# Kernel optimization log

Measured on AMD Instinct MI355X. Metric: run time of the kernel, lower is better.

The kernel has to match this reference:

```python
import jax, jax.numpy as jnp
import numpy as np

EPS = 1e-5

def layer_norm(x, g, b):
    mu = jnp.mean(x, axis=-1, keepdims=True)
    var = jnp.var(x, axis=-1, keepdims=True)
    return (x - mu) * jax.lax.rsqrt(var + EPS) * g + b

def setup_inputs() -> dict:
    key = jax.random.key(0)
    ks = jax.random.split(key, 8)
    B, N, C, H = 4, 1024, 1024, 16
    Dh = C * 4
    std = 0.02
    return {
        "x": jax.random.normal(ks[0], (B, N, C), dtype=jnp.float32),
        "qkv_w": jax.random.normal(ks[1], (3 * C, C), dtype=jnp.float32) * std,
        "proj_w": jax.random.normal(ks[2], (C, C), dtype=jnp.float32) * std,
        "proj_b": jnp.zeros((C,), dtype=jnp.float32),
        "fc1_w": jax.random.normal(ks[3], (Dh, C), dtype=jnp.float32) * std,
        "fc1_b": jnp.zeros((Dh,), dtype=jnp.float32),
        "fc2_w": jax.random.normal(ks[4], (C, Dh), dtype=jnp.float32) * std,
        "fc2_b": jnp.zeros((C,), dtype=jnp.float32),
        "ln1_g": jnp.ones((C,), dtype=jnp.float32),
        "ln1_b": jnp.zeros((C,), dtype=jnp.float32),
        "ln2_g": jnp.ones((C,), dtype=jnp.float32),
        "ln2_b": jnp.zeros((C,), dtype=jnp.float32),
        "lnh_g": jnp.ones((Dh,), dtype=jnp.float32),
        "lnh_b": jnp.zeros((Dh,), dtype=jnp.float32),
    }

def reference(x, qkv_w, proj_w, proj_b, fc1_w, fc1_b, fc2_w, fc2_b,
              ln1_g, ln1_b, ln2_g, ln2_b, lnh_g, lnh_b):
    B, N, C = x.shape
    H = 16
    Dh = C // H
    scale = Dh ** (-0.5)

    # --- attention sublayer (pre-norm) ---
    h = layer_norm(x, ln1_g, ln1_b)
    qkv = (h @ qkv_w.T).reshape(B, N, 3, H, Dh).transpose(2, 0, 3, 1, 4)  # [3,B,H,N,Dh]
    q, k, v = qkv[0], qkv[1], qkv[2]
    attn = jnp.einsum('bhid,bhjd->bhij', q, k) * scale
    attn = jax.nn.softmax(attn, axis=-1)
    o = jnp.einsum('bhij,bhjd->bhid', attn, v)          # [B,H,N,Dh]
    o = o.transpose(0, 2, 1, 3).reshape(B, N, C)
    o = o @ proj_w.T + proj_b
    x = x + o

    # --- MLP sublayer (pre-norm, with LN on hidden per use_ln=True) ---
    h = layer_norm(x, ln2_g, ln2_b)
    u = jax.nn.gelu(h @ fc1_w.T + fc1_b, approximate=False)  # torch nn.GELU = erf form
    u = layer_norm(u, lnh_g, lnh_b)
    m = u @ fc2_w.T + fc2_b
    return x + m
```

## Files before the change

### kernel.cpp

```cpp
#include <hip/hip_runtime.h>
#include <hip/hip_bf16.h>
#include <math.h>


#define TOKENS 4096
#define CDIM   1024
#define HEADS  16
#define DHEAD  64
#define HID    4096

typedef __attribute__((ext_vector_type(4))) float  floatx4;
typedef __attribute__((ext_vector_type(8))) short  short8;

__device__ __forceinline__ void gl_lds16(const void* g, void* l)
{
    __builtin_amdgcn_global_load_lds(
        (const __attribute__((address_space(1))) unsigned int*)g,
        (__attribute__((address_space(3))) unsigned int*)l,
        16, 0, 0);
}

__global__ __launch_bounds__(256) void cvt_all(
    const float* __restrict__ s0, const float* __restrict__ s1,
    const float* __restrict__ s2, const float* __restrict__ s3,
    __hip_bfloat16* __restrict__ dst)
{
    long i = (long)blockIdx.x * 256 + threadIdx.x;
    const float* src;
    long base;
    if (i < 768l * 1024)       { src = s0; base = 0; }
    else if (i < 1792l * 1024) { src = s1; base = 768l * 1024; }
    else if (i < 2816l * 1024) { src = s2; base = 1792l * 1024; }
    else                       { src = s3; base = 2816l * 1024; }
    float4 v = ((const float4*)src)[i - base];
    __hip_bfloat16 t[4];
    t[0] = __float2bfloat16(v.x);
    t[1] = __float2bfloat16(v.y);
    t[2] = __float2bfloat16(v.z);
    t[3] = __float2bfloat16(v.w);
    *(uint2*)(dst + 4l * i) = *(uint2*)t;
}

__global__ __launch_bounds__(256) void ln_f32_kernel(
    const float* __restrict__ x, const float* __restrict__ g,
    const float* __restrict__ b, __hip_bfloat16* __restrict__ y, int C)
{
    int row = blockIdx.x;
    const float4* xr = (const float4*)(x + (long)row * C);
    uint2* yr = (uint2*)(y + (long)row * C);
    const int C4 = C >> 2;

    float s = 0.f, ss = 0.f;
    for (int i = threadIdx.x; i < C4; i += 256) {
        float4 v = xr[i];
        s  += v.x + v.y + v.z + v.w;
        ss += v.x * v.x + v.y * v.y + v.z * v.z + v.w * v.w;
    }
    #pragma unroll
    for (int d = 32; d; d >>= 1) {
        s  += __shfl_down(s, d);
        ss += __shfl_down(ss, d);
    }
    __shared__ float buf[4][2];
    int wid = threadIdx.x >> 6, lane = threadIdx.x & 63;
    if (lane == 0) { buf[wid][0] = s; buf[wid][1] = ss; }
    __syncthreads();
    if (threadIdx.x == 0) {
        s = buf[0][0] + buf[1][0] + buf[2][0] + buf[3][0];
        ss = buf[0][1] + buf[1][1] + buf[2][1] + buf[3][1];
        buf[0][0] = s; buf[0][1] = ss;
    }
    __syncthreads();
    s = buf[0][0]; ss = buf[0][1];

    float invC = 1.f / (float)C;
    float mu = s * invC;
    float var = ss * invC - mu * mu;
    float inv = rsqrtf(var + 1e-5f);
    const float4* gg = (const float4*)g;
    const float4* bb = (const float4*)b;
    for (int i = threadIdx.x; i < C4; i += 256) {
        float4 v = xr[i], gv = gg[i], bv = bb[i];
        __hip_bfloat16 t[4];
        t[0] = __float2bfloat16((v.x - mu) * inv * gv.x + bv.x);
        t[1] = __float2bfloat16((v.y - mu) * inv * gv.y + bv.y);
        t[2] = __float2bfloat16((v.z - mu) * inv * gv.z + bv.z);
        t[3] = __float2bfloat16((v.w - mu) * inv * gv.w + bv.w);
        yr[i] = *(uint2*)t;
    }
}

__global__ __launch_bounds__(256) void ln_bf16_kernel(
    const __hip_bfloat16* __restrict__ x, const float* __restrict__ g,
    const float* __restrict__ b, __hip_bfloat16* __restrict__ y, int C)
{
    int row = blockIdx.x;
    const uint4* xr = (const uint4*)(x + (long)row * C);
    uint4* yr = (uint4*)(y + (long)row * C);
    const int C8 = C >> 3;

    float s = 0.f, ss = 0.f;
    for (int i = threadIdx.x; i < C8; i += 256) {
        uint4 raw = xr[i];
        const __hip_bfloat16* p = (const __hip_bfloat16*)&raw;
        #pragma unroll
        for (int j = 0; j < 8; ++j) {
            float v = __bfloat162float(p[j]);
            s += v; ss += v * v;
        }
    }
    #pragma unroll
    for (int d = 32; d; d >>= 1) {
        s  += __shfl_down(s, d);
        ss += __shfl_down(ss, d);
    }
    __shared__ float buf[4][2];
    int wid = threadIdx.x >> 6, lane = threadIdx.x & 63;
    if (lane == 0) { buf[wid][0] = s; buf[wid][1] = ss; }
    __syncthreads();
    if (threadIdx.x == 0) {
        s = buf[0][0] + buf[1][0] + buf[2][0] + buf[3][0];
        ss = buf[0][1] + buf[1][1] + buf[2][1] + buf[3][1];
        buf[0][0] = s; buf[0][1] = ss;
    }
    __syncthreads();
    s = buf[0][0]; ss = buf[0][1];

    float invC = 1.f / (float)C;
    float mu = s * invC;
    float var = ss * invC - mu * mu;
    float inv = rsqrtf(var + 1e-5f);
    const float4* gg = (const float4*)g;
    const float4* bb = (const float4*)b;
    for (int i = threadIdx.x; i < C8; i += 256) {
        uint4 raw = xr[i];
        const __hip_bfloat16* p = (const __hip_bfloat16*)&raw;
        float4 g0 = gg[2 * i], g1 = gg[2 * i + 1];
        float4 b0 = bb[2 * i], b1 = bb[2 * i + 1];
        __hip_bfloat16 t[8];
        t[0] = __float2bfloat16((__bfloat162float(p[0]) - mu) * inv * g0.x + b0.x);
        t[1] = __float2bfloat16((__bfloat162float(p[1]) - mu) * inv * g0.y + b0.y);
        t[2] = __float2bfloat16((__bfloat162float(p[2]) - mu) * inv * g0.z + b0.z);
        t[3] = __float2bfloat16((__bfloat162float(p[3]) - mu) * inv * g0.w + b0.w);
        t[4] = __float2bfloat16((__bfloat162float(p[4]) - mu) * inv * g1.x + b1.x);
        t[5] = __float2bfloat16((__bfloat162float(p[5]) - mu) * inv * g1.y + b1.y);
        t[6] = __float2bfloat16((__bfloat162float(p[6]) - mu) * inv * g1.z + b1.z);
        t[7] = __float2bfloat16((__bfloat162float(p[7]) - mu) * inv * g1.w + b1.w);
        yr[i] = *(uint4*)t;
    }
}

template<int BK>
__global__ __launch_bounds__(256, BK == 64 ? 2 : 1) void gemm_db(
    const __hip_bfloat16* __restrict__ A,
    const __hip_bfloat16* __restrict__ W,
    const float* __restrict__ bias, const float* __restrict__ residual,
    void* __restrict__ Cout, int M, int N, int K, int mode)
{
    constexpr int ROWSEG = 512 / BK;
    constexpr int CHK    = BK / 8;
    constexpr int MASK   = CHK - 1;
    constexpr int NSEGW  = BK / 16;
    constexpr int RS     = 2 * BK;
    constexpr int KH     = BK / 32;

    __shared__ __align__(16) char Asl[2][BK * 256];
    __shared__ __align__(16) char Bsl[2][BK * 256];

    int tid = threadIdx.x;
    int wave = tid >> 6, lane = tid & 63;

    int mt, nt;
    {
        int gx = gridDim.x, gy = gridDim.y;
        int lin = blockIdx.y * gx + blockIdx.x;
        int chunk = gy >> 3;
        int xcd = lin & 7, q = lin >> 3;
        mt = xcd * chunk + (q % chunk);
        nt = q / chunk;
    }
    int bm = mt * 128, bn = nt * 128;
    int wm = wave & 1, wn = wave >> 1;
    int fm = lane & 15, quad = lane >> 4;

    const int nk = K / BK;

    const int rsub  = lane / CHK;
    const int cphys = lane & MASK;
    const __hip_bfloat16* gA[NSEGW];
    const __hip_bfloat16* gB[NSEGW];
    int dseg[NSEGW];
    #pragma unroll
    for (int j = 0; j < NSEGW; ++j) {
        int seg = wave * NSEGW + j;
        int row = seg * ROWSEG + rsub;
        int csrc = cphys ^ (row & MASK);
        gA[j] = A + (long)(bm + row) * K + csrc * 8;
        gB[j] = W + (long)(bn + row) * K + csrc * 8;
        dseg[j] = seg * 1024;
    }

#define STAGE(b, kt) { \
    const long ko = (long)(kt) * BK; \
    _Pragma("unroll") \
    for (int j = 0; j < NSEGW; ++j) { \
        gl_lds16(gA[j] + ko, Asl[b] + dseg[j]); \
        gl_lds16(gB[j] + ko, Bsl[b] + dseg[j]); \
    } }

    floatx4 acc[4][4] = {};

    STAGE(0, 0);
    __syncthreads();

    int cur = 0;
    for (int kt = 0; kt < nk; ++kt) {
        if (kt + 1 < nk) STAGE(cur ^ 1, kt + 1);

        const char* Ab = Asl[cur];
        const char* Bb = Bsl[cur];
        #pragma unroll
        for (int kh = 0; kh < KH; ++kh) {
            const int xsw = (((kh * 4 + quad) ^ (fm & MASK)) << 4);
            short8 bq[4];
            #pragma unroll
            for (int j = 0; j < 4; ++j)
                bq[j] = *(const short8*)(Bb + (wn * 64 + j * 16 + fm) * RS + xsw);
            #pragma unroll
            for (int i = 0; i < 4; ++i) {
                short8 af = *(const short8*)(Ab + (wm * 64 + i * 16 + fm) * RS + xsw);
                #pragma unroll
                for (int j = 0; j < 4; ++j)
                    acc[i][j] = __builtin_amdgcn_mfma_f32_16x16x32_bf16(
                        af, bq[j], acc[i][j], 0, 0, 0);
            }
        }
        __syncthreads();
        cur ^= 1;
    }
#undef STAGE

    int mbase = bm + wm * 64;
    int nbase = bn + wn * 64;
    if (mode == 2) {
        float* Cf = (float*)Cout;
        #pragma unroll
        for (int i = 0; i < 4; ++i) {
            #pragma unroll
            for (int j = 0; j < 4; ++j) {
                int ncol = nbase + j * 16 + fm;
                float bv = bias[ncol];
                #pragma unroll
                for (int r = 0; r < 4; ++r) {
                    int mrow = mbase + i * 16 + quad * 4 + r;
                    long idx = (long)mrow * N + ncol;
                    Cf[idx] = acc[i][j][r] + bv + residual[idx];
                }
            }
        }
    } else {
        __hip_bfloat16* Cb = (__hip_bfloat16*)Cout;
        #pragma unroll
        for (int i = 0; i < 4; ++i) {
            #pragma unroll
            for (int j = 0; j < 4; ++j) {
                int ncol = nbase + j * 16 + fm;
                #pragma unroll
                for (int r = 0; r < 4; ++r) {
                    int mrow = mbase + i * 16 + quad * 4 + r;
                    float v = acc[i][j][r];
                    if (bias) v += bias[ncol];
                    if (mode == 1) {
                        float z = v * (1.5957691216f + 0.0713548162f * v * v);
                        v = v / (1.f + __expf(-z));
                    }
                    Cb[(long)mrow * N + ncol] = __float2bfloat16(v);
                }
            }
        }
    }
}

__global__ __launch_bounds__(256) void attn_mfma(
    const __hip_bfloat16* __restrict__ qkv, __hip_bfloat16* __restrict__ o_out)
{
    __shared__ __align__(16) char Ks[2][64 * 144];
    __shared__ __align__(16) char Vt[2][64 * 144];
    __shared__ __align__(16) char Ps[4 * 16 * 144];

    const int C3 = 3 * CDIM;
    int lin = blockIdx.x;
    int xcd = lin & 7, q = lin >> 3;
    int bh = xcd * 8 + (q >> 4);
    int qt = q & 15;
    int b = bh >> 4, hh = bh & 15;
    int tid = threadIdx.x, wave = tid >> 6, lane = tid & 63;
    int l = lane & 15, quad = lane >> 4;

    const __hip_bfloat16* qrow =
        qkv + (long)(b * 1024 + qt * 64 + wave * 16 + l) * C3 + hh * DHEAD;
    short8 qf0 = *(const short8*)(qrow + quad * 8);
    short8 qf1 = *(const short8*)(qrow + 32 + quad * 8);

    char* Psw = Ps + wave * (16 * 144);

    int sc = tid & 7;
    int skl = tid >> 3;

    const __hip_bfloat16* Kbase = qkv + (long)(b * 1024) * C3 + CDIM + hh * DHEAD;
    const __hip_bfloat16* Vbase = qkv + (long)(b * 1024) * C3 + 2 * CDIM + hh * DHEAD;
    const int kpp = skl ^ (sc << 2);

    floatx4 facc[4] = {};
    float mrun = -1e30f, lrun = 0.f;

    uint4 kA0, kA1, vA0, vA1;
    uint4 kB0, kB1, vB0, vB1;

#define GKV(t, k0, k1, v0, v1) { \
    const __hip_bfloat16* Kg = Kbase + (long)((t) * 64) * C3; \
    const __hip_bfloat16* Vg = Vbase + (long)((t) * 64) * C3; \
    k0 = *(const uint4*)(Kg + (long)skl * C3 + sc * 8); \
    k1 = *(const uint4*)(Kg + (long)(skl + 32) * C3 + sc * 8); \
    v0 = *(const uint4*)(Vg + (long)(2 * skl) * C3 + sc * 8); \
    v1 = *(const uint4*)(Vg + (long)(2 * skl + 1) * C3 + sc * 8); }
#define WKV(bf, k0, k1, v0, v1) { \
    *(uint4*)(Ks[bf] + skl * 144 + sc * 16) = k0; \
    *(uint4*)(Ks[bf] + (skl + 32) * 144 + sc * 16) = k1; \
    const ushort* e0 = (const ushort*)&v0; \
    const ushort* e1 = (const ushort*)&v1; \
    _Pragma("unroll") \
    for (int j = 0; j < 8; ++j) { \
        unsigned dw = (unsigned)e0[j] | ((unsigned)e1[j] << 16); \
        *(unsigned*)(Vt[bf] + (sc * 8 + j) * 144 + kpp * 4) = dw; \
    } }

    auto compute = [&](int buf) {
        floatx4 st[4] = {};
        #pragma unroll
        for (int kb = 0; kb < 4; ++kb) {
            short8 k0 = *(const short8*)(Ks[buf] + (kb * 16 + l) * 144 + quad * 16);
            short8 k1 = *(const short8*)(Ks[buf] + (kb * 16 + l) * 144 + 64 + quad * 16);
            st[kb] = __builtin_amdgcn_mfma_f32_16x16x32_bf16(k0, qf0, st[kb], 0, 0, 0);
            st[kb] = __builtin_amdgcn_mfma_f32_16x16x32_bf16(k1, qf1, st[kb], 0, 0, 0);
        }
        float p[16];
        float tm = -1e30f;
        #pragma unroll
        for (int kb = 0; kb < 4; ++kb)
            #pragma unroll
            for (int r = 0; r < 4; ++r) {
                float s = st[kb][r] * 0.125f;
                p[kb * 4 + r] = s;
                tm = fmaxf(tm, s);
            }
        tm = fmaxf(tm, __shfl_xor(tm, 16));
        tm = fmaxf(tm, __shfl_xor(tm, 32));
        float mn = fmaxf(mrun, tm);
        float alpha = __expf(mrun - mn);
        float psum = 0.f;
        #pragma unroll
        for (int i = 0; i < 16; ++i) { p[i] = __expf(p[i] - mn); psum += p[i]; }
        psum += __shfl_xor(psum, 16);
        psum += __shfl_xor(psum, 32);
        lrun = lrun * alpha + psum;
        mrun = mn;

        #pragma unroll
        for (int kb = 0; kb < 4; ++kb) {
            __hip_bfloat16 t[4];
            #pragma unroll
            for (int r = 0; r < 4; ++r) t[r] = __float2bfloat16(p[kb * 4 + r]);
            *(uint2*)(Psw + l * 144 + kb * 32 + quad * 8) = *(const uint2*)t;
        }

        float a0 = __shfl(alpha, quad * 4 + 0);
        float a1 = __shfl(alpha, quad * 4 + 1);
        float a2 = __shfl(alpha, quad * 4 + 2);
        float a3 = __shfl(alpha, quad * 4 + 3);
        #pragma unroll
        for (int db = 0; db < 4; ++db) {
            facc[db][0] *= a0; facc[db][1] *= a1;
            facc[db][2] *= a2; facc[db][3] *= a3;
        }

        short8 pf0 = *(const short8*)(Psw + l * 144 + quad * 16);
        short8 pf1 = *(const short8*)(Psw + l * 144 + 64 + quad * 16);
        #pragma unroll
        for (int db = 0; db < 4; ++db) {
            int d = db * 16 + l;
            int o3 = (d >> 3) & 7;
            short8 v0 = *(const short8*)(Vt[buf] + d * 144 + ((quad ^ o3) << 4));
            short8 v1 = *(const short8*)(Vt[buf] + d * 144 + (((4 + quad) ^ o3) << 4));
            facc[db] = __builtin_amdgcn_mfma_f32_16x16x32_bf16(pf0, v0, facc[db], 0, 0, 0);
            facc[db] = __builtin_amdgcn_mfma_f32_16x16x32_bf16(pf1, v1, facc[db], 0, 0, 0);
        }
    };

    GKV(0, kA0, kA1, vA0, vA1);
    #pragma unroll 1
    for (int kt = 0; kt < 16; kt += 2) {
        WKV(0, kA0, kA1, vA0, vA1);
        __syncthreads();
        GKV(kt + 1, kB0, kB1, vB0, vB1);
        compute(0);
        WKV(1, kB0, kB1, vB0, vB1);
        __syncthreads();
        if (kt + 2 < 16) GKV(kt + 2, kA0, kA1, vA0, vA1);
        compute(1);
    }
#undef GKV
#undef WKV

    float il0 = 1.f / __shfl(lrun, quad * 4 + 0);
    float il1 = 1.f / __shfl(lrun, quad * 4 + 1);
    float il2 = 1.f / __shfl(lrun, quad * 4 + 2);
    float il3 = 1.f / __shfl(lrun, quad * 4 + 3);
    __hip_bfloat16* orow =
        o_out + (long)(b * 1024 + qt * 64 + wave * 16) * CDIM + hh * DHEAD;
    #pragma unroll
    for (int db = 0; db < 4; ++db) {
        int col = db * 16 + l;
        orow[(quad * 4 + 0) * CDIM + col] = __float2bfloat16(facc[db][0] * il0);
        orow[(quad * 4 + 1) * CDIM + col] = __float2bfloat16(facc[db][1] * il1);
        orow[(quad * 4 + 2) * CDIM + col] = __float2bfloat16(facc[db][2] * il2);
        orow[(quad * 4 + 3) * CDIM + col] = __float2bfloat16(facc[db][3] * il3);
    }
}

extern "C" void kernel_launch(void* const* d_in, const int* in_sizes, int n_in,
                              void* d_out, int out_size, void* d_ws, size_t ws_size,
                              hipStream_t stream)
{
    const float* x      = (const float*)d_in[0];
    const float* qkv_w  = (const float*)d_in[1];
    const float* proj_w = (const float*)d_in[2];
    const float* proj_b = (const float*)d_in[3];
    const float* fc1_w  = (const float*)d_in[4];
    const float* fc1_b  = (const float*)d_in[5];
    const float* fc2_w  = (const float*)d_in[6];
    const float* fc2_b  = (const float*)d_in[7];
    const float* ln1_g  = (const float*)d_in[8];
    const float* ln1_b  = (const float*)d_in[9];
    const float* ln2_g  = (const float*)d_in[10];
    const float* ln2_b  = (const float*)d_in[11];
    const float* lnh_g  = (const float*)d_in[12];
    const float* lnh_b  = (const float*)d_in[13];

    float* out = (float*)d_out;

    __hip_bfloat16* wsb     = (__hip_bfloat16*)d_ws;
    __hip_bfloat16* qkvw_bf = wsb;
    __hip_bfloat16* fc1w_bf = qkvw_bf + 3l * 1024 * 1024;
    __hip_bfloat16* fc2w_bf = fc1w_bf + 4l * 1024 * 1024;
    __hip_bfloat16* projw_bf= fc2w_bf + 4l * 1024 * 1024;
    __hip_bfloat16* h_bf    = projw_bf + 1l * 1024 * 1024;
    __hip_bfloat16* qkv_bf  = h_bf + 4l * 1024 * 1024;
    __hip_bfloat16* o_bf    = qkv_bf + 12l * 1024 * 1024;
    __hip_bfloat16* u_bf    = o_bf + 4l * 1024 * 1024;

    cvt_all<<<12288, 256, 0, stream>>>(qkv_w, fc1_w, fc2_w, proj_w, qkvw_bf);

    ln_f32_kernel<<<TOKENS, 256, 0, stream>>>(x, ln1_g, ln1_b, h_bf, CDIM);
    gemm_db<64><<<dim3(3072 / 128, TOKENS / 128), 256, 0, stream>>>(
        h_bf, qkvw_bf, nullptr, nullptr, qkv_bf, TOKENS, 3072, CDIM, 0);
    attn_mfma<<<1024, 256, 0, stream>>>(qkv_bf, o_bf);
    gemm_db<128><<<dim3(CDIM / 128, TOKENS / 128), 256, 0, stream>>>(
        o_bf, projw_bf, proj_b, x, out, TOKENS, CDIM, CDIM, 2);
    ln_f32_kernel<<<TOKENS, 256, 0, stream>>>(out, ln2_g, ln2_b, h_bf, CDIM);
    gemm_db<64><<<dim3(HID / 128, TOKENS / 128), 256, 0, stream>>>(
        h_bf, fc1w_bf, fc1_b, nullptr, u_bf, TOKENS, HID, CDIM, 1);
    ln_bf16_kernel<<<TOKENS, 256, 0, stream>>>(u_bf, lnh_g, lnh_b, u_bf, HID);
    gemm_db<128><<<dim3(CDIM / 128, TOKENS / 128), 256, 0, stream>>>(
        u_bf, fc2w_bf, fc2_b, out, out, TOKENS, CDIM, HID, 2);
}
```

Baseline: 373.5 us.

## Add 256x256-tile 8-wave GEMM for QKV and FC1 projections

Adds a new bf16 MFMA GEMM kernel with 512 threads (8 waves) and a 256x256 output tile. It double-buffers K=64 slices as two 32-wide halves through direct global-to-LDS loads, uses an XOR-swizzled LDS layout, and remaps blocks so each XCD works on a contiguous band of rows. The QKV and FC1 GEMMs now use it instead of the 128x128 gemm_db, aiming for more reuse per tile and better L2 locality. The tradeoff is larger register and LDS use per block (a 128-float accumulator per thread) and fewer blocks (192 and 256), which may underfill the device.

```diff
diff --git a/kernel.cpp b/kernel.cpp
--- a/kernel.cpp
+++ b/kernel.cpp
@@ -150,6 +150,114 @@
     }
 }
 
+__global__ __launch_bounds__(512, 2) void gemm8p(
+    const __hip_bfloat16* __restrict__ A,
+    const __hip_bfloat16* __restrict__ W,
+    const float* __restrict__ bias,
+    __hip_bfloat16* __restrict__ Cout, int M, int N, int K, int mode)
+{
+    __shared__ __align__(16) char Lds[2][2][2][16384];
+
+    const int tid = threadIdx.x;
+    const int wave = tid >> 6, lane = tid & 63;
+    const int fm = lane & 15, quad = lane >> 4;
+
+    int mt, nt;
+    {
+        int gx = gridDim.x, gy = gridDim.y;
+        int lin = blockIdx.y * gx + blockIdx.x;
+        int chunk = gy >> 3;
+        int xcd = lin & 7, q = lin >> 3;
+        mt = xcd * chunk + (q % chunk);
+        nt = q / chunk;
+    }
+    const int bm = mt * 256, bn = nt * 256;
+    const int wm = wave >> 2, wn = wave & 3;
+
+    const int nk = K / 64;
+
+    const int clog = (lane & 3) ^ ((lane >> 3) & 3);
+    const int srow = wave * 16 + (lane >> 2);
+    const __hip_bfloat16* gAb = A + (long)(bm + srow) * K + clog * 8;
+    const __hip_bfloat16* gBb = W + (long)(bn + srow) * K + clog * 8;
+    const long rK = (long)128 * K;
+    const int ldst = wave * 1024;
+
+#define STAGE8(b, kt, h) { \
+    const long go = (long)(kt) * 64 + (h) * 32; \
+    gl_lds16(gAb + go,      &Lds[b][0][h][ldst]); \
+    gl_lds16(gAb + rK + go, &Lds[b][0][h][8192 + ldst]); \
+    gl_lds16(gBb + go,      &Lds[b][1][h][ldst]); \
+    gl_lds16(gBb + rK + go, &Lds[b][1][h][8192 + ldst]); }
+
+    const int rdoff = fm * 64 + ((quad ^ ((fm >> 1) & 3)) << 4);
+
+    floatx4 acc[8][4] = {};
+
+    STAGE8(0, 0, 0);
+    STAGE8(0, 0, 1);
+    asm volatile("s_waitcnt vmcnt(4)" ::: "memory");
+    __builtin_amdgcn_s_barrier();
+    __builtin_amdgcn_sched_barrier(0);
+
+    #pragma unroll 1
+    for (int t = 0; t < nk; ++t) {
+        const int c = t & 1;
+        #pragma unroll
+        for (int h = 0; h < 2; ++h) {
+            if (t + 1 < nk) STAGE8(c ^ 1, t + 1, h);
+
+            const char* As = Lds[c][0][h];
+            const char* Bs = Lds[c][1][h];
+            short8 bq[4];
+            #pragma unroll
+            for (int j = 0; j < 4; ++j)
+                bq[j] = *(const short8*)(Bs + (wn * 64 + j * 16) * 64 + rdoff);
+
+            __builtin_amdgcn_s_setprio(1);
+            #pragma unroll
+            for (int i = 0; i < 8; ++i) {
+                short8 af = *(const short8*)(As + (wm * 128 + i * 16) * 64 + rdoff);
+                #pragma unroll
+                for (int j = 0; j < 4; ++j)
+                    acc[i][j] = __builtin_amdgcn_mfma_f32_16x16x32_bf16(
+                        af, bq[j], acc[i][j], 0, 0, 0);
+            }
+            __builtin_amdgcn_s_setprio(0);
+
+            if (t + 1 < nk) {
+                asm volatile("s_waitcnt vmcnt(4)" ::: "memory");
+            } else if (h == 0) {
+                asm volatile("s_waitcnt vmcnt(0)" ::: "memory");
+            }
+            __builtin_amdgcn_s_barrier();
+            __builtin_amdgcn_sched_barrier(0);
+        }
+    }
+#undef STAGE8
+
+    const int mbase = bm + wm * 128;
+    const int nbase = bn + wn * 64;
+    #pragma unroll
+    for (int i = 0; i < 8; ++i) {
+        #pragma unroll
+        for (int j = 0; j < 4; ++j) {
+            int ncol = nbase + j * 16 + fm;
+            #pragma unroll
+            for (int r = 0; r < 4; ++r) {
+                int mrow = mbase + i * 16 + quad * 4 + r;
+                float v = acc[i][j][r];
+                if (bias) v += bias[ncol];
+                if (mode == 1) {
+                    float z = v * (1.5957691216f + 0.0713548162f * v * v);
+                    v = v / (1.f + __expf(-z));
+                }
+                Cout[(long)mrow * N + ncol] = __float2bfloat16(v);
+            }
+        }
+    }
+}
+
 template<int BK>
 __global__ __launch_bounds__(256, BK == 64 ? 2 : 1) void gemm_db(
     const __hip_bfloat16* __restrict__ A,
@@ -462,14 +570,14 @@
     cvt_all<<<12288, 256, 0, stream>>>(qkv_w, fc1_w, fc2_w, proj_w, qkvw_bf);
 
     ln_f32_kernel<<<TOKENS, 256, 0, stream>>>(x, ln1_g, ln1_b, h_bf, CDIM);
-    gemm_db<64><<<dim3(3072 / 128, TOKENS / 128), 256, 0, stream>>>(
-        h_bf, qkvw_bf, nullptr, nullptr, qkv_bf, TOKENS, 3072, CDIM, 0);
+    gemm8p<<<dim3(3072 / 256, TOKENS / 256), 512, 0, stream>>>(
+        h_bf, qkvw_bf, nullptr, qkv_bf, TOKENS, 3072, CDIM, 0);
     attn_mfma<<<1024, 256, 0, stream>>>(qkv_bf, o_bf);
     gemm_db<128><<<dim3(CDIM / 128, TOKENS / 128), 256, 0, stream>>>(
         o_bf, projw_bf, proj_b, x, out, TOKENS, CDIM, CDIM, 2);
     ln_f32_kernel<<<TOKENS, 256, 0, stream>>>(out, ln2_g, ln2_b, h_bf, CDIM);
-    gemm_db<64><<<dim3(HID / 128, TOKENS / 128), 256, 0, stream>>>(
-        h_bf, fc1w_bf, fc1_b, nullptr, u_bf, TOKENS, HID, CDIM, 1);
+    gemm8p<<<dim3(HID / 256, TOKENS / 256), 512, 0, stream>>>(
+        h_bf, fc1w_bf, fc1_b, u_bf, TOKENS, HID, CDIM, 1);
     ln_bf16_kernel<<<TOKENS, 256, 0, stream>>>(u_bf, lnh_g, lnh_b, u_bf, HID);
     gemm_db<128><<<dim3(CDIM / 128, TOKENS / 128), 256, 0, stream>>>(
         u_bf, fc2w_bf, fc2_b, out, out, TOKENS, CDIM, HID, 2);
```

After: 358.0 us. 1.04x faster.
